# Kernel optimization log

Measured on AMD Instinct MI355X. Metric: run time of the kernel, lower is better.

## Reference

```python
import jax, jax.numpy as jnp
import numpy as np

B, M, A, F = 8, 512, 16, 128  # batch, atoms/messages, irrep dim (n_ang_mom**2=16), feature channels
CG_DENSITY = 0.25             # CG coefficient tensors are highly sparse; emulate with a random mask


def setup_inputs() -> dict:
    key = jax.random.key(0)
    kx, ky, kc, km = jax.random.split(key, 4)
    x = jax.random.normal(kx, (B, M, A, F), dtype=jnp.float32)
    y = jax.random.normal(ky, (B, M, A, F), dtype=jnp.float32)
    # stand-in for cgc_multiplier(n_ang_mom): sparse [a, d, c] Clebsch-Gordan coefficient tensor
    cgc_dense = jax.random.normal(kc, (A, A, A), dtype=jnp.float32)
    mask = jax.random.bernoulli(km, CG_DENSITY, (A, A, A))
    cgc = jnp.where(mask, cgc_dense, 0.0)
    return {"x": x, "y": y, "cgc": cgc}


def reference(x, y, cgc):
    # TensorProductContractionLayer.call: triple contraction over irrep indices a, c
    # x: [b,m,a,f], y: [b,m,c,f], cgc: [a,d,c] -> res: [b,m,d,f]
    return jnp.einsum('bmaf,bmcf,adc->bmdf', x, y, cgc)
```

## Files before the change

kernel.cpp:

```cpp
#include <hip/hip_runtime.h>


typedef __attribute__((ext_vector_type(2))) _Float16 half2v;
typedef __attribute__((ext_vector_type(8))) _Float16 half8;
typedef __attribute__((ext_vector_type(4))) float    floatx4;
typedef __attribute__((ext_vector_type(2))) float    float2v;

#define AA 16
#define FF 128

union H8 { half2v h2[4]; half8 h8; };

static __device__ __forceinline__ half2v pkrtz(float a, float b) {
    return __builtin_bit_cast(half2v, __builtin_amdgcn_cvt_pkrtz(a, b));
}

__global__ __launch_bounds__(256, 4)
void tpc_mfma_pair_kernel(const float* __restrict__ x,
                          const float* __restrict__ y,
                          const float* __restrict__ cgc,
                          float* __restrict__ out) {
    const int tid  = threadIdx.x;
    const int w    = tid >> 6;
    const int lane = tid & 63;
    const int L    = lane & 15;
    const int quad = lane >> 4;
    const int qh   = quad >> 1;
    const int c0   = (quad & 1) * 8;

    const int bm = blockIdx.x * 4 + w;
    const size_t stride = (size_t)(AA * FF);
    const float* xb = x + (size_t)bm * stride;
    const float* yb = y + (size_t)bm * stride;
    float*       ob = out + (size_t)bm * stride;

    float2v xv[8], yv[8];
#pragma unroll
    for (int t = 0; t < 8; ++t)
        xv[t] = *(const float2v*)(xb + (2 * t + qh) * FF + 2 * L);
#pragma unroll
    for (int j = 0; j < 8; ++j)
        yv[j] = *(const float2v*)(yb + (c0 + j) * FF + 2 * L);

    half8 wfrag[8];
#pragma unroll
    for (int t = 0; t < 8; ++t) {
        const float* wp = cgc + (2 * t + qh) * (AA * AA) + L * AA + c0;
        const floatx4 w0 = *(const floatx4*)(wp);
        const floatx4 w1 = *(const floatx4*)(wp + 4);
        H8 wa;
        wa.h2[0] = pkrtz(w0.x, w0.y);
        wa.h2[1] = pkrtz(w0.z, w0.w);
        wa.h2[2] = pkrtz(w1.x, w1.y);
        wa.h2[3] = pkrtz(w1.z, w1.w);
        wfrag[t] = wa.h8;
    }

    for (int g = 0; g < 4; ++g) {
        half2v yp0[4], yp1[4];
#pragma unroll
        for (int jj = 0; jj < 4; ++jj) {
            yp0[jj] = pkrtz(yv[2 * jj].x, yv[2 * jj + 1].x);
            yp1[jj] = pkrtz(yv[2 * jj].y, yv[2 * jj + 1].y);
        }
        half2v xp0[8], xp1[8];
#pragma unroll
        for (int t = 0; t < 8; ++t) {
            xp0[t] = pkrtz(xv[t].x, xv[t].x);
            xp1[t] = pkrtz(xv[t].y, xv[t].y);
        }

        if (g < 3) {
            const int fA = (g + 1) * 32 + 2 * L;
#pragma unroll
            for (int t = 0; t < 8; ++t)
                xv[t] = *(const float2v*)(xb + (2 * t + qh) * FF + fA);
#pragma unroll
            for (int j = 0; j < 8; ++j)
                yv[j] = *(const float2v*)(yb + (c0 + j) * FF + fA);
        }

        floatx4 acc0 = {0.f, 0.f, 0.f, 0.f};
        floatx4 acc1 = {0.f, 0.f, 0.f, 0.f};
#pragma unroll
        for (int t = 0; t < 8; ++t) {
            H8 b0;
            b0.h2[0] = xp0[t] * yp0[0];
            b0.h2[1] = xp0[t] * yp0[1];
            b0.h2[2] = xp0[t] * yp0[2];
            b0.h2[3] = xp0[t] * yp0[3];
            acc0 = __builtin_amdgcn_mfma_f32_16x16x32_f16(wfrag[t], b0.h8, acc0, 0, 0, 0);

            H8 b1;
            b1.h2[0] = xp1[t] * yp1[0];
            b1.h2[1] = xp1[t] * yp1[1];
            b1.h2[2] = xp1[t] * yp1[2];
            b1.h2[3] = xp1[t] * yp1[3];
            acc1 = __builtin_amdgcn_mfma_f32_16x16x32_f16(wfrag[t], b1.h8, acc1, 0, 0, 0);
        }

        const int f0 = g * 32 + 2 * L;
#pragma unroll
        for (int r = 0; r < 4; ++r) {
            const int row = (quad * 4 + r) * FF;
            float2v v = { acc0[r], acc1[r] };
            *(float2v*)(ob + row + f0) = v;
        }
    }
}

extern "C" void kernel_launch(void* const* d_in, const int* in_sizes, int n_in,
                              void* d_out, int out_size, void* d_ws, size_t ws_size,
                              hipStream_t stream) {
    const float* x   = (const float*)d_in[0];
    const float* y   = (const float*)d_in[1];
    const float* cgc = (const float*)d_in[2];
    float* out = (float*)d_out;

    hipLaunchKernelGGL(tpc_mfma_pair_kernel, dim3(1024), dim3(256), 0, stream,
                       x, y, cgc, out);
}
```

Before: 110.0 us.

## Split each (b,m) across two waves and raise occupancy to eight blocks

Each wave now handles half of the feature dimension for one (b,m) pair, and the grid doubles to 2048 blocks with launch bounds raised to 8 blocks per CU. Per-wave state shrinks: the CG weight fragments are reloaded from cache inside the loop instead of held in registers, the paired float2 loads and dual accumulators become scalar loads with one accumulator, and the explicit next-group prefetch is dropped. The aim is to hide memory latency through more resident waves rather than software prefetch, at the cost of narrower 4-byte memory accesses and repeated weight loads and conversions.

```diff
diff --git a/kernel.cpp b/kernel.cpp
--- a/kernel.cpp
+++ b/kernel.cpp
@@ -4,7 +4,6 @@
 typedef __attribute__((ext_vector_type(2))) _Float16 half2v;
 typedef __attribute__((ext_vector_type(8))) _Float16 half8;
 typedef __attribute__((ext_vector_type(4))) float    floatx4;
-typedef __attribute__((ext_vector_type(2))) float    float2v;
 
 #define AA 16
 #define FF 128
@@ -15,8 +14,8 @@
     return __builtin_bit_cast(half2v, __builtin_amdgcn_cvt_pkrtz(a, b));
 }
 
-__global__ __launch_bounds__(256, 4)
-void tpc_mfma_pair_kernel(const float* __restrict__ x,
+__global__ __launch_bounds__(256, 8)
+void tpc_mfma_occ8_kernel(const float* __restrict__ x,
                           const float* __restrict__ y,
                           const float* __restrict__ cgc,
                           float* __restrict__ out) {
@@ -28,83 +27,60 @@
     const int qh   = quad >> 1;
     const int c0   = (quad & 1) * 8;
 
-    const int bm = blockIdx.x * 4 + w;
+    const int bm    = blockIdx.x * 2 + (w >> 1);
+    const int fbase = (w & 1) * 64;
+
     const size_t stride = (size_t)(AA * FF);
-    const float* xb = x + (size_t)bm * stride;
-    const float* yb = y + (size_t)bm * stride;
-    float*       ob = out + (size_t)bm * stride;
+    const float* xb = x + (size_t)bm * stride + fbase;
+    const float* yb = y + (size_t)bm * stride + fbase;
+    float*       ob = out + (size_t)bm * stride + fbase;
+    const float* wbase = cgc + qh * (AA * AA) + L * AA + c0;
 
-    float2v xv[8], yv[8];
 #pragma unroll
-    for (int t = 0; t < 8; ++t)
-        xv[t] = *(const float2v*)(xb + (2 * t + qh) * FF + 2 * L);
+    for (int g = 0; g < 4; ++g) {
+        const int f0 = g * 16 + L;
+
+        float xv[8], yv[8];
 #pragma unroll
-    for (int j = 0; j < 8; ++j)
-        yv[j] = *(const float2v*)(yb + (c0 + j) * FF + 2 * L);
+        for (int t = 0; t < 8; ++t)
+            xv[t] = xb[(2 * t + qh) * FF + f0];
+#pragma unroll
+        for (int j = 0; j < 8; ++j)
+            yv[j] = yb[(c0 + j) * FF + f0];
 
-    half8 wfrag[8];
+        half2v yp[4];
 #pragma unroll
-    for (int t = 0; t < 8; ++t) {
-        const float* wp = cgc + (2 * t + qh) * (AA * AA) + L * AA + c0;
-        const floatx4 w0 = *(const floatx4*)(wp);
-        const floatx4 w1 = *(const floatx4*)(wp + 4);
-        H8 wa;
-        wa.h2[0] = pkrtz(w0.x, w0.y);
-        wa.h2[1] = pkrtz(w0.z, w0.w);
-        wa.h2[2] = pkrtz(w1.x, w1.y);
-        wa.h2[3] = pkrtz(w1.z, w1.w);
-        wfrag[t] = wa.h8;
-    }
+        for (int jj = 0; jj < 4; ++jj)
+            yp[jj] = pkrtz(yv[2 * jj], yv[2 * jj + 1]);
+        half2v xp[8];
+#pragma unroll
+        for (int t = 0; t < 8; ++t)
+            xp[t] = pkrtz(xv[t], xv[t]);
 
-    for (int g = 0; g < 4; ++g) {
-        half2v yp0[4], yp1[4];
-#pragma unroll
-        for (int jj = 0; jj < 4; ++jj) {
-            yp0[jj] = pkrtz(yv[2 * jj].x, yv[2 * jj + 1].x);
-            yp1[jj] = pkrtz(yv[2 * jj].y, yv[2 * jj + 1].y);
-        }
-        half2v xp0[8], xp1[8];
+        floatx4 acc = {0.f, 0.f, 0.f, 0.f};
 #pragma unroll
         for (int t = 0; t < 8; ++t) {
-            xp0[t] = pkrtz(xv[t].x, xv[t].x);
-            xp1[t] = pkrtz(xv[t].y, xv[t].y);
+            const float* wp = wbase + t * (2 * AA * AA);
+            const floatx4 w0 = *(const floatx4*)(wp);
+            const floatx4 w1 = *(const floatx4*)(wp + 4);
+            H8 wa;
+            wa.h2[0] = pkrtz(w0.x, w0.y);
+            wa.h2[1] = pkrtz(w0.z, w0.w);
+            wa.h2[2] = pkrtz(w1.x, w1.y);
+            wa.h2[3] = pkrtz(w1.z, w1.w);
+
+            H8 b;
+            b.h2[0] = xp[t] * yp[0];
+            b.h2[1] = xp[t] * yp[1];
+            b.h2[2] = xp[t] * yp[2];
+            b.h2[3] = xp[t] * yp[3];
+            acc = __builtin_amdgcn_mfma_f32_16x16x32_f16(wa.h8, b.h8, acc, 0, 0, 0);
         }
 
-        if (g < 3) {
-            const int fA = (g + 1) * 32 + 2 * L;
-#pragma unroll
-            for (int t = 0; t < 8; ++t)
-                xv[t] = *(const float2v*)(xb + (2 * t + qh) * FF + fA);
-#pragma unroll
-            for (int j = 0; j < 8; ++j)
-                yv[j] = *(const float2v*)(yb + (c0 + j) * FF + fA);
-        }
-
-        floatx4 acc0 = {0.f, 0.f, 0.f, 0.f};
-        floatx4 acc1 = {0.f, 0.f, 0.f, 0.f};
-#pragma unroll
-        for (int t = 0; t < 8; ++t) {
-            H8 b0;
-            b0.h2[0] = xp0[t] * yp0[0];
-            b0.h2[1] = xp0[t] * yp0[1];
-            b0.h2[2] = xp0[t] * yp0[2];
-            b0.h2[3] = xp0[t] * yp0[3];
-            acc0 = __builtin_amdgcn_mfma_f32_16x16x32_f16(wfrag[t], b0.h8, acc0, 0, 0, 0);
-
-            H8 b1;
-            b1.h2[0] = xp1[t] * yp1[0];
-            b1.h2[1] = xp1[t] * yp1[1];
-            b1.h2[2] = xp1[t] * yp1[2];
-            b1.h2[3] = xp1[t] * yp1[3];
-            acc1 = __builtin_amdgcn_mfma_f32_16x16x32_f16(wfrag[t], b1.h8, acc1, 0, 0, 0);
-        }
-
-        const int f0 = g * 32 + 2 * L;
 #pragma unroll
         for (int r = 0; r < 4; ++r) {
             const int row = (quad * 4 + r) * FF;
-            float2v v = { acc0[r], acc1[r] };
-            *(float2v*)(ob + row + f0) = v;
+            ob[row + f0] = acc[r];
         }
     }
 }
@@ -117,6 +93,6 @@
     const float* cgc = (const float*)d_in[2];
     float* out = (float*)d_out;
 
-    hipLaunchKernelGGL(tpc_mfma_pair_kernel, dim3(1024), dim3(256), 0, stream,
+    hipLaunchKernelGGL(tpc_mfma_occ8_kernel, dim3(2048), dim3(256), 0, stream,
                        x, y, cgc, out);
 }
```

Result: slower. 122.4 us (+11.3%).

## Stage x/y through triple-buffered LDS with async global-to-LDS loads

Applied to the files above, without the earlier changes.

Each block now handles 8 consecutive (b,m) slices instead of one per wave. The four waves split the feature dimension, and input tiles are prefetched two slices ahead into a triple-buffered LDS ring using global_load_lds. Explicit vmcnt waits plus barriers sequence the pipeline, so loads for later slices overlap the MFMA work of the current one. In exchange, occupancy is lower because of the LDS use and the launch bounds of 2, output stores become scalar, and the hand-tuned vmcnt counts depend on stores being counted in vmcnt.

```diff
diff --git a/kernel.cpp b/kernel.cpp
--- a/kernel.cpp
+++ b/kernel.cpp
@@ -4,10 +4,11 @@
 typedef __attribute__((ext_vector_type(2))) _Float16 half2v;
 typedef __attribute__((ext_vector_type(8))) _Float16 half8;
 typedef __attribute__((ext_vector_type(4))) float    floatx4;
-typedef __attribute__((ext_vector_type(2))) float    float2v;
 
 #define AA 16
 #define FF 128
+#define BM_PER_BLOCK 8
+#define NBUF 3
 
 union H8 { half2v h2[4]; half8 h8; };
 
@@ -15,11 +16,28 @@
     return __builtin_bit_cast(half2v, __builtin_amdgcn_cvt_pkrtz(a, b));
 }
 
-__global__ __launch_bounds__(256, 4)
-void tpc_mfma_pair_kernel(const float* __restrict__ x,
-                          const float* __restrict__ y,
-                          const float* __restrict__ cgc,
-                          float* __restrict__ out) {
+static __device__ __forceinline__ void gload_lds16(const float* g, float* l) {
+    __builtin_amdgcn_global_load_lds(
+        (const __attribute__((address_space(1))) void*)g,
+        (__attribute__((address_space(3))) void*)l,
+        16, 0, 0);
+}
+
+#define WAITB(N) do {                                            \
+    asm volatile("s_waitcnt vmcnt(" #N ")" ::: "memory");        \
+    __builtin_amdgcn_sched_barrier(0);                           \
+    __builtin_amdgcn_s_barrier();                                \
+    __builtin_amdgcn_sched_barrier(0);                           \
+} while (0)
+
+__global__ __launch_bounds__(256, 2)
+void tpc_mfma_vmcnt_kernel(const float* __restrict__ x,
+                           const float* __restrict__ y,
+                           const float* __restrict__ cgc,
+                           float* __restrict__ out) {
+    __shared__ float lx[NBUF][AA * FF];
+    __shared__ float ly[NBUF][AA * FF];
+
     const int tid  = threadIdx.x;
     const int w    = tid >> 6;
     const int lane = tid & 63;
@@ -28,19 +46,24 @@
     const int qh   = quad >> 1;
     const int c0   = (quad & 1) * 8;
 
-    const int bm = blockIdx.x * 4 + w;
+    const int bm0 = blockIdx.x * BM_PER_BLOCK;
     const size_t stride = (size_t)(AA * FF);
-    const float* xb = x + (size_t)bm * stride;
-    const float* yb = y + (size_t)bm * stride;
-    float*       ob = out + (size_t)bm * stride;
+    const int off = w * 512 + lane * 4;
+    const int f0  = w * 32 + L;
 
-    float2v xv[8], yv[8];
-#pragma unroll
-    for (int t = 0; t < 8; ++t)
-        xv[t] = *(const float2v*)(xb + (2 * t + qh) * FF + 2 * L);
-#pragma unroll
-    for (int j = 0; j < 8; ++j)
-        yv[j] = *(const float2v*)(yb + (c0 + j) * FF + 2 * L);
+    auto STAGE = [&](int i) {
+        const float* xb = x + (size_t)(bm0 + i) * stride;
+        const float* yb = y + (size_t)(bm0 + i) * stride;
+        float* lxd = &lx[i % NBUF][0];
+        float* lyd = &ly[i % NBUF][0];
+        gload_lds16(xb + off,       lxd + off);
+        gload_lds16(xb + off + 256, lxd + off + 256);
+        gload_lds16(yb + off,       lyd + off);
+        gload_lds16(yb + off + 256, lyd + off + 256);
+    };
+
+    STAGE(0);
+    STAGE(1);
 
     half8 wfrag[8];
 #pragma unroll
@@ -56,57 +79,69 @@
         wfrag[t] = wa.h8;
     }
 
-    for (int g = 0; g < 4; ++g) {
-        half2v yp0[4], yp1[4];
+    auto COMPUTE = [&](int i) {
+        const float* lxc = &lx[i % NBUF][0];
+        const float* lyc = &ly[i % NBUF][0];
+
+        float xvA[8], xvB[8], yvA[8], yvB[8];
+#pragma unroll
+        for (int j = 0; j < 8; ++j) {
+            yvA[j] = lyc[(c0 + j) * FF + f0];
+            yvB[j] = lyc[(c0 + j) * FF + f0 + 16];
+        }
+#pragma unroll
+        for (int t = 0; t < 8; ++t) {
+            xvA[t] = lxc[(2 * t + qh) * FF + f0];
+            xvB[t] = lxc[(2 * t + qh) * FF + f0 + 16];
+        }
+
+        half2v ypA[4], ypB[4];
 #pragma unroll
         for (int jj = 0; jj < 4; ++jj) {
-            yp0[jj] = pkrtz(yv[2 * jj].x, yv[2 * jj + 1].x);
-            yp1[jj] = pkrtz(yv[2 * jj].y, yv[2 * jj + 1].y);
-        }
-        half2v xp0[8], xp1[8];
-#pragma unroll
-        for (int t = 0; t < 8; ++t) {
-            xp0[t] = pkrtz(xv[t].x, xv[t].x);
-            xp1[t] = pkrtz(xv[t].y, xv[t].y);
-        }
-
-        if (g < 3) {
-            const int fA = (g + 1) * 32 + 2 * L;
-#pragma unroll
-            for (int t = 0; t < 8; ++t)
-                xv[t] = *(const float2v*)(xb + (2 * t + qh) * FF + fA);
-#pragma unroll
-            for (int j = 0; j < 8; ++j)
-                yv[j] = *(const float2v*)(yb + (c0 + j) * FF + fA);
+            ypA[jj] = pkrtz(yvA[2 * jj], yvA[2 * jj + 1]);
+            ypB[jj] = pkrtz(yvB[2 * jj], yvB[2 * jj + 1]);
         }
 
         floatx4 acc0 = {0.f, 0.f, 0.f, 0.f};
         floatx4 acc1 = {0.f, 0.f, 0.f, 0.f};
 #pragma unroll
         for (int t = 0; t < 8; ++t) {
+            half2v xp = pkrtz(xvA[t], xvA[t]);
             H8 b0;
-            b0.h2[0] = xp0[t] * yp0[0];
-            b0.h2[1] = xp0[t] * yp0[1];
-            b0.h2[2] = xp0[t] * yp0[2];
-            b0.h2[3] = xp0[t] * yp0[3];
+            b0.h2[0] = xp * ypA[0];
+            b0.h2[1] = xp * ypA[1];
+            b0.h2[2] = xp * ypA[2];
+            b0.h2[3] = xp * ypA[3];
             acc0 = __builtin_amdgcn_mfma_f32_16x16x32_f16(wfrag[t], b0.h8, acc0, 0, 0, 0);
 
+            xp = pkrtz(xvB[t], xvB[t]);
             H8 b1;
-            b1.h2[0] = xp1[t] * yp1[0];
-            b1.h2[1] = xp1[t] * yp1[1];
-            b1.h2[2] = xp1[t] * yp1[2];
-            b1.h2[3] = xp1[t] * yp1[3];
+            b1.h2[0] = xp * ypB[0];
+            b1.h2[1] = xp * ypB[1];
+            b1.h2[2] = xp * ypB[2];
+            b1.h2[3] = xp * ypB[3];
             acc1 = __builtin_amdgcn_mfma_f32_16x16x32_f16(wfrag[t], b1.h8, acc1, 0, 0, 0);
         }
 
-        const int f0 = g * 32 + 2 * L;
+        float* ob = out + (size_t)(bm0 + i) * stride;
 #pragma unroll
         for (int r = 0; r < 4; ++r) {
             const int row = (quad * 4 + r) * FF;
-            float2v v = { acc0[r], acc1[r] };
-            *(float2v*)(ob + row + f0) = v;
+            ob[row + f0]      = acc0[r];
+            ob[row + f0 + 16] = acc1[r];
         }
-    }
+    };
+
+#define BODY(i, N) do { WAITB(N); COMPUTE(i); if ((i) + 2 < BM_PER_BLOCK) STAGE((i) + 2); } while (0)
+    BODY(0, 4);
+    BODY(1, 12);
+    BODY(2, 12);
+    BODY(3, 12);
+    BODY(4, 12);
+    BODY(5, 12);
+    BODY(6, 12);
+    BODY(7, 8);
+#undef BODY
 }
 
 extern "C" void kernel_launch(void* const* d_in, const int* in_sizes, int n_in,
@@ -117,6 +152,6 @@
     const float* cgc = (const float*)d_in[2];
     float* out = (float*)d_out;
 
-    hipLaunchKernelGGL(tpc_mfma_pair_kernel, dim3(1024), dim3(256), 0, stream,
+    hipLaunchKernelGGL(tpc_mfma_vmcnt_kernel, dim3(512), dim3(256), 0, stream,
                        x, y, cgc, out);
 }
```

Measured after the change: 106.4 us. 1.03x faster.
